# Performance work log

Hardware: AMD Instinct MI355X
Metric: run time of the kernel (lower is better)

Reference implementation:

```python
import jax, jax.numpy as jnp
import numpy as np

N_NODES = 50000


def setup_inputs() -> dict:
    key = jax.random.key(0)
    ks = jax.random.split(key, 6)
    E = 640000
    H = 128
    data = jax.random.normal(ks[0], (N_NODES, H), dtype=jnp.float32)
    edge = jax.random.randint(ks[1], (2, E), 0, N_NODES, dtype=jnp.int64)
    att = jax.random.uniform(ks[2], (E,), dtype=jnp.float32)
    w1 = jax.random.normal(ks[3], (2 * H, H), dtype=jnp.float32) * (1.0 / np.sqrt(2 * H))
    b1 = jnp.zeros((H,), dtype=jnp.float32)
    w2 = jax.random.normal(ks[4], (2 * H, H), dtype=jnp.float32) * (1.0 / np.sqrt(2 * H))
    b2 = jnp.zeros((H,), dtype=jnp.float32)
    return {"data": data, "edge": edge, "att": att, "w1": w1, "b1": b1, "w2": w2, "b2": b2}


def _simple_conv_mean_cat(x, edge, att):
    # PyG SimpleConv(aggr='mean', combine_root='cat') with scalar edge weights.
    src, dst = edge[0], edge[1]
    msgs = x[src] * att[:, None]                               # [E, H] gather + scale
    summed = jax.ops.segment_sum(msgs, dst, num_segments=N_NODES)   # [N, H]
    deg = jax.ops.segment_sum(jnp.ones_like(att), dst, num_segments=N_NODES)  # [N]
    agg = summed / jnp.maximum(deg, 1.0)[:, None]              # mean over incoming edges
    return jnp.concatenate([x, agg], axis=-1)                  # [N, 2H]


def reference(data, edge, att, w1, b1, w2, b2):
    out = _simple_conv_mean_cat(data, edge, att)
    out = jax.nn.relu(out @ w1 + b1)
    out = _simple_conv_mean_cat(out, edge, att)
    out = jax.nn.relu(out @ w2 + b2)
    return out
```

## Files before the change

### kernel.cpp

```cpp
#include <hip/hip_runtime.h>


#define HDIM 128
#define CAP 32
#define FCH 2048

typedef __bf16 bf16x8 __attribute__((ext_vector_type(8)));
typedef float floatx4 __attribute__((ext_vector_type(4)));

__device__ __forceinline__ unsigned short f2bf(float f) {
    unsigned int u = __float_as_uint(f);
    unsigned int r = (u + 0x7fff + ((u >> 16) & 1)) >> 16;
    return (unsigned short)r;
}
__device__ __forceinline__ float bf2f(unsigned short b) {
    return __uint_as_float((unsigned int)b << 16);
}
__device__ __forceinline__ void acc8(const uint4& u, float a, float* s) {
    s[0] = fmaf(bf2f((unsigned short)(u.x & 0xffff)), a, s[0]);
    s[1] = fmaf(bf2f((unsigned short)(u.x >> 16)), a, s[1]);
    s[2] = fmaf(bf2f((unsigned short)(u.y & 0xffff)), a, s[2]);
    s[3] = fmaf(bf2f((unsigned short)(u.y >> 16)), a, s[3]);
    s[4] = fmaf(bf2f((unsigned short)(u.z & 0xffff)), a, s[4]);
    s[5] = fmaf(bf2f((unsigned short)(u.z >> 16)), a, s[5]);
    s[6] = fmaf(bf2f((unsigned short)(u.w & 0xffff)), a, s[6]);
    s[7] = fmaf(bf2f((unsigned short)(u.w >> 16)), a, s[7]);
}

__global__ __launch_bounds__(256) void k_fill(const int* __restrict__ edge, int E,
                                              const float* __restrict__ att,
                                              int* __restrict__ cursor,
                                              int* __restrict__ ovf_cnt,
                                              unsigned int* __restrict__ pse,
                                              float4* __restrict__ ovf, int rsize,
                                              int nfb,
                                              const float* __restrict__ data,
                                              unsigned short* __restrict__ data_bf, int n4,
                                              int cb, int NN,
                                              const float* __restrict__ w1,
                                              unsigned short* __restrict__ w1s,
                                              const float* __restrict__ w2,
                                              unsigned short* __restrict__ w2s) {
    int b = blockIdx.x;
    int t = threadIdx.x;
    if (b < nfb) {
        __shared__ int s_or;
        if (t == 0) s_or = 0;
        __syncthreads();
        int nw = 2 * E < 512 ? 2 * E : 512;
        int iw = t * 2 + 1;
        int vw = (iw < nw) ? edge[iw] : 0;
        if (vw != 0) atomicOr(&s_or, 1);
        __syncthreads();
        int sh = (s_or == 0) ? 1 : 0;

        int r = b & 7;
        int c = b >> 3;
        int lo = r * rsize;
        int hi = lo + rsize;
        int e0 = c * FCH;
        int ds[8];
#pragma unroll
        for (int k = 0; k < 8; ++k) {
            int e = e0 + t + k * 256;
            ds[k] = (e < E) ? edge[(size_t)(E + e) << sh] : -1;
        }
#pragma unroll
        for (int k = 0; k < 8; ++k) {
            int d = ds[k];
            if (d >= lo && d < hi) {
                int e = e0 + t + k * 256;
                int s = edge[(size_t)e << sh];
                float a = att[e];
                int slot = atomicAdd(&cursor[d], 1);
                if (slot < CAP) {
                    unsigned int rec = ((unsigned int)f2bf(a) << 16) | (unsigned int)(s & 0xffff);
                    pse[(size_t)d * CAP + slot] = rec;
                } else {
                    int oi = atomicAdd(ovf_cnt, 1);
                    ovf[oi] = make_float4(__int_as_float(d), __int_as_float(s), a, 0.f);
                }
            }
        }
        return;
    }
    b -= nfb;
    if (b < cb) {
        int i = b * 256 + t;
        if (i < n4) {
            float4 v = ((const float4*)data)[i];
            ushort4 o;
            o.x = f2bf(v.x); o.y = f2bf(v.y); o.z = f2bf(v.z); o.w = f2bf(v.w);
            int nn = i >> 5;
            int c4 = i & 31;
            *(ushort4*)(data_bf + (((size_t)(c4 >> 3) * NN + nn) << 5) + ((c4 & 7) << 2)) = o;
        }
        return;
    }
    b -= cb;
    {
        const float* w = (b < 128) ? w1 : w2;
        unsigned short* wt = (b < 128) ? w1s : w2s;
        int bb = (b < 128) ? b : b - 128;
        int idx = bb * 256 + t;
        int k = idx >> 7;
        int n = idx & 127;
        int c = n >> 4, l16 = n & 15;
        int kc = k >> 5, quad = (k >> 3) & 3, j = k & 7;
        int lane = quad * 16 + l16;
        size_t f = (((size_t)(c * 8 + kc) * 64 + lane) << 3) + j;
        wt[f] = f2bf(w[(size_t)k * 128 + n]);
    }
}

__global__ __launch_bounds__(256, 4) void k_layer(const unsigned short* __restrict__ x,
                                                  const unsigned int* __restrict__ pse,
                                                  const int* __restrict__ cursor,
                                                  const int* __restrict__ ovf_cnt,
                                                  const float4* __restrict__ ovf,
                                                  const unsigned short* __restrict__ Wsw,
                                                  const float* __restrict__ bias,
                                                  float* __restrict__ outF,
                                                  unsigned short* __restrict__ outB,
                                                  int M) {
    __shared__ __align__(16) unsigned int s_rec[64 * 36];
    __shared__ __align__(16) unsigned short s_agg[64 * 136];
    int tid = threadIdx.x;
    int base = blockIdx.x * 64;

#pragma unroll
    for (int k = 0; k < 2; ++k) {
        int idx4 = tid + k * 256;
        int i = idx4 >> 3;
        int j0 = (idx4 & 7) << 2;
        int nn = base + i;
        uint4 v = make_uint4(0u, 0u, 0u, 0u);
        if (nn < M) v = *(const uint4*)(pse + ((size_t)nn << 5) + j0);
        *(uint4*)(&s_rec[i * 36 + j0]) = v;
    }
    __syncthreads();

    int lane = tid & 63;
    int wave = tid >> 6;
    int q = lane >> 2;
    int l4 = lane & 3;
    int ni = wave * 16 + q;
    int n = base + ni;
    bool valid = n < M;
    int deg = valid ? cursor[n] : 0;
    int m = min(deg, CAP);
    const unsigned int* rp = &s_rec[ni * 36];
    float inv = 1.0f / fmaxf((float)deg, 1.0f);
    int oc = ovf_cnt[0];

    for (int pass = 0; pass < 4; ++pass) {
        const unsigned short* xs = x + (((size_t)pass * M) << 5) + (l4 << 3);
        float s[8] = {0.f, 0.f, 0.f, 0.f, 0.f, 0.f, 0.f, 0.f};

        for (int j = 0; j < m; j += 16) {
            unsigned int rr[16];
#pragma unroll
            for (int k = 0; k < 16; ++k) {
                unsigned int r = rp[j + k];
                rr[k] = (j + k < m) ? r : 0u;
            }
            uint4 uu[16];
#pragma unroll
            for (int k = 0; k < 16; ++k)
                uu[k] = *(const uint4*)(xs + ((size_t)(rr[k] & 0xffffu) << 5));
#pragma unroll
            for (int k = 0; k < 16; ++k)
                acc8(uu[k], __uint_as_float(rr[k] & 0xffff0000u), s);
        }

        if (oc > 0 && valid) {
            for (int k = 0; k < oc; ++k) {
                float4 f = ovf[k];
                if (__float_as_int(f.x) == n) {
                    uint4 u2 = *(const uint4*)(xs + ((size_t)__float_as_int(f.y) << 5));
                    acc8(u2, f.z, s);
                }
            }
        }

        uint4 o;
        o.x = (unsigned int)f2bf(s[0] * inv) | ((unsigned int)f2bf(s[1] * inv) << 16);
        o.y = (unsigned int)f2bf(s[2] * inv) | ((unsigned int)f2bf(s[3] * inv) << 16);
        o.z = (unsigned int)f2bf(s[4] * inv) | ((unsigned int)f2bf(s[5] * inv) << 16);
        o.w = (unsigned int)f2bf(s[6] * inv) | ((unsigned int)f2bf(s[7] * inv) << 16);
        *(uint4*)(&s_agg[ni * 136 + pass * 32 + l4 * 8]) = o;
    }
    __syncthreads();

    int l16 = lane & 15;
    int quad = lane >> 4;
    int row = base + wave * 16 + l16;
    int rowA = min(row, M - 1);
    int lrow = wave * 16 + l16;
    const unsigned short* xb0 = x + ((size_t)rowA << 5) + quad * 8;
    bf16x8 af[8];
#pragma unroll
    for (int kc = 0; kc < 4; ++kc) af[kc] = *(const bf16x8*)(xb0 + (((size_t)kc * M) << 5));
#pragma unroll
    for (int kc = 0; kc < 4; ++kc)
        af[kc + 4] = *(const bf16x8*)(&s_agg[lrow * 136 + kc * 32 + quad * 8]);

    floatx4 acc[8];
#pragma unroll
    for (int c = 0; c < 8; ++c) acc[c] = (floatx4){0.f, 0.f, 0.f, 0.f};

#pragma unroll
    for (int kc = 0; kc < 8; ++kc) {
#pragma unroll
        for (int c = 0; c < 8; ++c) {
            bf16x8 bfr = *(const bf16x8*)(Wsw + (((size_t)(c * 8 + kc) * 64 + lane) << 3));
            acc[c] = __builtin_amdgcn_mfma_f32_16x16x32_bf16(af[kc], bfr, acc[c], 0, 0, 0);
        }
    }

    int orow0 = base + wave * 16 + quad * 4;
#pragma unroll
    for (int c = 0; c < 8; ++c) {
        int col = c * 16 + l16;
        float bv = bias[col];
#pragma unroll
        for (int r = 0; r < 4; ++r) {
            int orow = orow0 + r;
            if (orow < M) {
                float v = fmaxf(acc[c][r] + bv, 0.f);
                if (outF) outF[(size_t)orow * 128 + col] = v;
                else outB[(((size_t)(col >> 5) * M + orow) << 5) + (col & 31)] = f2bf(v);
            }
        }
    }
}

extern "C" void kernel_launch(void* const* d_in, const int* in_sizes, int n_in,
                              void* d_out, int out_size, void* d_ws, size_t ws_size,
                              hipStream_t stream) {
    const float* data = (const float*)d_in[0];
    const int* edge = (const int*)d_in[1];
    const float* att = (const float*)d_in[2];
    const float* w1 = (const float*)d_in[3];
    const float* b1 = (const float*)d_in[4];
    const float* w2 = (const float*)d_in[5];
    const float* b2 = (const float*)d_in[6];

    const int N = in_sizes[0] / HDIM;
    const int E = in_sizes[1] / 2;

    char* ws = (char*)d_ws;
    size_t o = 0;
    auto carve = [&](size_t bytes) -> char* {
        char* r = ws + o;
        o = (o + bytes + 255) & ~(size_t)255;
        return r;
    };
    int* cursor = (int*)carve((size_t)(N + 4) * 4);
    int* ovf_cnt = cursor + N;
    unsigned int* pse = (unsigned int*)carve((size_t)N * CAP * 4);
    float4* ovf = (float4*)carve((size_t)E * 16);
    unsigned short* data_bf = (unsigned short*)carve((size_t)N * 128 * 2);
    unsigned short* w1s = (unsigned short*)carve(256 * 128 * 2);
    unsigned short* w2s = (unsigned short*)carve(256 * 128 * 2);
    unsigned short* out1_bf = (unsigned short*)carve((size_t)N * 128 * 2);
    float* outF = (float*)d_out;

    hipMemsetAsync(cursor, 0, (size_t)(N + 4) * 4, stream);

    int rsize = (N + 7) / 8;
    int nch = (E + FCH - 1) / FCH;
    int nfb = nch * 8;
    int n4 = N * 32;
    int cb = (n4 + 255) / 256;
    k_fill<<<nfb + cb + 256, 256, 0, stream>>>(edge, E, att, cursor, ovf_cnt, pse, ovf,
                                               rsize, nfb, data, data_bf, n4, cb, N,
                                               w1, w1s, w2, w2s);

    int nbk = (N + 63) / 64;
    k_layer<<<nbk, 256, 0, stream>>>(data_bf, pse, cursor, ovf_cnt, ovf,
                                     w1s, b1, nullptr, out1_bf, N);
    k_layer<<<nbk, 256, 0, stream>>>(out1_bf, pse, cursor, ovf_cnt, ovf,
                                     w2s, b2, outF, nullptr, N);
}
```

Before: 206.1 us.

## Shrink layer block to 16 nodes, spread feature passes and output columns across waves

Each block now handles 16 nodes instead of 64. The four feature-chunk passes of the gather run in parallel across thread groups instead of as a sequential loop per thread, and each wave computes 2 of the 8 output column tiles of the MFMA GEMM. The aim is more independent memory requests in flight, better latency hiding, and more blocks for load balance. The cost is four times as many blocks, and every block reloads the weight fragments, which adds weight traffic and per-block overhead.

```diff
diff --git a/kernel.cpp b/kernel.cpp
--- a/kernel.cpp
+++ b/kernel.cpp
@@ -4,6 +4,7 @@
 #define HDIM 128
 #define CAP 32
 #define FCH 2048
+#define NPB 16
 
 typedef __bf16 bf16x8 __attribute__((ext_vector_type(8)));
 typedef float floatx4 __attribute__((ext_vector_type(4)));
@@ -123,16 +124,14 @@
                                                   float* __restrict__ outF,
                                                   unsigned short* __restrict__ outB,
                                                   int M) {
-    __shared__ __align__(16) unsigned int s_rec[64 * 36];
-    __shared__ __align__(16) unsigned short s_agg[64 * 136];
+    __shared__ __align__(16) unsigned int s_rec[NPB * 36];
+    __shared__ __align__(16) unsigned short s_agg[NPB * 136];
     int tid = threadIdx.x;
-    int base = blockIdx.x * 64;
-
-#pragma unroll
-    for (int k = 0; k < 2; ++k) {
-        int idx4 = tid + k * 256;
-        int i = idx4 >> 3;
-        int j0 = (idx4 & 7) << 2;
+    int base = blockIdx.x * NPB;
+
+    if (tid < NPB * 8) {
+        int i = tid >> 3;
+        int j0 = (tid & 7) << 2;
         int nn = base + i;
         uint4 v = make_uint4(0u, 0u, 0u, 0u);
         if (nn < M) v = *(const uint4*)(pse + ((size_t)nn << 5) + j0);
@@ -140,11 +139,10 @@
     }
     __syncthreads();
 
-    int lane = tid & 63;
-    int wave = tid >> 6;
-    int q = lane >> 2;
-    int l4 = lane & 3;
-    int ni = wave * 16 + q;
+    int g = tid >> 2;
+    int l4 = tid & 3;
+    int ni = g & (NPB - 1);
+    int pass = g >> 4;
     int n = base + ni;
     bool valid = n < M;
     int deg = valid ? cursor[n] : 0;
@@ -153,36 +151,36 @@
     float inv = 1.0f / fmaxf((float)deg, 1.0f);
     int oc = ovf_cnt[0];
 
-    for (int pass = 0; pass < 4; ++pass) {
-        const unsigned short* xs = x + (((size_t)pass * M) << 5) + (l4 << 3);
-        float s[8] = {0.f, 0.f, 0.f, 0.f, 0.f, 0.f, 0.f, 0.f};
-
-        for (int j = 0; j < m; j += 16) {
-            unsigned int rr[16];
-#pragma unroll
-            for (int k = 0; k < 16; ++k) {
-                unsigned int r = rp[j + k];
-                rr[k] = (j + k < m) ? r : 0u;
+    const unsigned short* xs = x + (((size_t)pass * M) << 5) + (l4 << 3);
+    float s[8] = {0.f, 0.f, 0.f, 0.f, 0.f, 0.f, 0.f, 0.f};
+
+    for (int j = 0; j < m; j += 16) {
+        unsigned int rr[16];
+#pragma unroll
+        for (int k = 0; k < 16; ++k) {
+            unsigned int r = rp[j + k];
+            rr[k] = (j + k < m) ? r : 0u;
+        }
+        uint4 uu[16];
+#pragma unroll
+        for (int k = 0; k < 16; ++k)
+            uu[k] = *(const uint4*)(xs + ((size_t)(rr[k] & 0xffffu) << 5));
+#pragma unroll
+        for (int k = 0; k < 16; ++k)
+            acc8(uu[k], __uint_as_float(rr[k] & 0xffff0000u), s);
+    }
+
+    if (oc > 0 && valid) {
+        for (int k = 0; k < oc; ++k) {
+            float4 f = ovf[k];
+            if (__float_as_int(f.x) == n) {
+                uint4 u2 = *(const uint4*)(xs + ((size_t)__float_as_int(f.y) << 5));
+                acc8(u2, f.z, s);
             }
-            uint4 uu[16];
-#pragma unroll
-            for (int k = 0; k < 16; ++k)
-                uu[k] = *(const uint4*)(xs + ((size_t)(rr[k] & 0xffffu) << 5));
-#pragma unroll
-            for (int k = 0; k < 16; ++k)
-                acc8(uu[k], __uint_as_float(rr[k] & 0xffff0000u), s);
-        }
-
-        if (oc > 0 && valid) {
-            for (int k = 0; k < oc; ++k) {
-                float4 f = ovf[k];
-                if (__float_as_int(f.x) == n) {
-                    uint4 u2 = *(const uint4*)(xs + ((size_t)__float_as_int(f.y) << 5));
-                    acc8(u2, f.z, s);
-                }
-            }
-        }
-
+        }
+    }
+
+    {
         uint4 o;
         o.x = (unsigned int)f2bf(s[0] * inv) | ((unsigned int)f2bf(s[1] * inv) << 16);
         o.y = (unsigned int)f2bf(s[2] * inv) | ((unsigned int)f2bf(s[3] * inv) << 16);
@@ -192,42 +190,43 @@
     }
     __syncthreads();
 
+    int lane = tid & 63;
+    int wave = tid >> 6;
     int l16 = lane & 15;
     int quad = lane >> 4;
-    int row = base + wave * 16 + l16;
-    int rowA = min(row, M - 1);
-    int lrow = wave * 16 + l16;
+    int rowA = min(base + l16, M - 1);
     const unsigned short* xb0 = x + ((size_t)rowA << 5) + quad * 8;
     bf16x8 af[8];
 #pragma unroll
     for (int kc = 0; kc < 4; ++kc) af[kc] = *(const bf16x8*)(xb0 + (((size_t)kc * M) << 5));
 #pragma unroll
     for (int kc = 0; kc < 4; ++kc)
-        af[kc + 4] = *(const bf16x8*)(&s_agg[lrow * 136 + kc * 32 + quad * 8]);
-
-    floatx4 acc[8];
-#pragma unroll
-    for (int c = 0; c < 8; ++c) acc[c] = (floatx4){0.f, 0.f, 0.f, 0.f};
+        af[kc + 4] = *(const bf16x8*)(&s_agg[l16 * 136 + kc * 32 + quad * 8]);
+
+    floatx4 acc[2];
+#pragma unroll
+    for (int ci = 0; ci < 2; ++ci) acc[ci] = (floatx4){0.f, 0.f, 0.f, 0.f};
 
 #pragma unroll
     for (int kc = 0; kc < 8; ++kc) {
 #pragma unroll
-        for (int c = 0; c < 8; ++c) {
+        for (int ci = 0; ci < 2; ++ci) {
+            int c = wave * 2 + ci;
             bf16x8 bfr = *(const bf16x8*)(Wsw + (((size_t)(c * 8 + kc) * 64 + lane) << 3));
-            acc[c] = __builtin_amdgcn_mfma_f32_16x16x32_bf16(af[kc], bfr, acc[c], 0, 0, 0);
-        }
-    }
-
-    int orow0 = base + wave * 16 + quad * 4;
-#pragma unroll
-    for (int c = 0; c < 8; ++c) {
-        int col = c * 16 + l16;
+            acc[ci] = __builtin_amdgcn_mfma_f32_16x16x32_bf16(af[kc], bfr, acc[ci], 0, 0, 0);
+        }
+    }
+
+    int orow0 = base + quad * 4;
+#pragma unroll
+    for (int ci = 0; ci < 2; ++ci) {
+        int col = (wave * 2 + ci) * 16 + l16;
         float bv = bias[col];
 #pragma unroll
         for (int r = 0; r < 4; ++r) {
             int orow = orow0 + r;
             if (orow < M) {
-                float v = fmaxf(acc[c][r] + bv, 0.f);
+                float v = fmaxf(acc[ci][r] + bv, 0.f);
                 if (outF) outF[(size_t)orow * 128 + col] = v;
                 else outB[(((size_t)(col >> 5) * M + orow) << 5) + (col & 31)] = f2bf(v);
             }
@@ -277,7 +276,7 @@
                                                rsize, nfb, data, data_bf, n4, cb, N,
                                                w1, w1s, w2, w2s);
 
-    int nbk = (N + 63) / 64;
+    int nbk = (N + NPB - 1) / NPB;
     k_layer<<<nbk, 256, 0, stream>>>(data_bf, pse, cursor, ovf_cnt, ovf,
                                      w1s, b1, nullptr, out1_bf, N);
     k_layer<<<nbk, 256, 0, stream>>>(out1_bf, pse, cursor, ovf_cnt, ovf,
```

Result: slower. 225.3 us (+9.3%).
